# Performance work log

Hardware: AMD Instinct MI355X
Metric: run time of the kernel (lower is better)

The kernel has to match this reference:

```python
import jax, jax.numpy as jnp
import numpy as np

B, T, E, H = 4, 4096, 1024, 16
D = E // H          # per-head hidden_size in fla LinearAttention (num_heads=1)
CH = 64             # fused-chunk chunk size


def setup_inputs() -> dict:
    key = jax.random.key(0)
    k1, k2, k3, k4, k5 = jax.random.split(key, 5)
    s = 1.0 / np.sqrt(D).astype(np.float32)
    x = jax.random.normal(k1, (B, T, E), dtype=jnp.float32)
    Wq = jax.random.normal(k2, (D, D), dtype=jnp.float32) * s
    Wk = jax.random.normal(k3, (D, D), dtype=jnp.float32) * s
    Wv = jax.random.normal(k4, (D, D), dtype=jnp.float32) * s
    Wo = jax.random.normal(k5, (D, D), dtype=jnp.float32) * s
    return {"x": x, "Wq": Wq, "Wk": Wk, "Wv": Wv, "Wo": Wo}


def _phi(x):
    # fla 'elu' feature map: elu(x) + 1 (positive features)
    return jax.nn.elu(x) + 1.0


def _linear_attn_fused_chunk(q, k, v):
    # q,k,v: [B,H,T,D]; causal linear attention via chunked recurrence.
    b, h, t, d = q.shape
    n = t // CH
    # [N, B, H, CH, D] so scan runs over chunks
    qc = q.reshape(b, h, n, CH, d).transpose(2, 0, 1, 3, 4)
    kc = k.reshape(b, h, n, CH, d).transpose(2, 0, 1, 3, 4)
    vc = v.reshape(b, h, n, CH, d).transpose(2, 0, 1, 3, 4)
    mask = jnp.tril(jnp.ones((CH, CH), dtype=q.dtype))  # causal, diag inclusive

    def step(S, inp):
        qi, ki, vi = inp                                   # [B,H,CH,D]
        attn = jnp.einsum('bhck,bhek->bhce', qi, ki) * mask  # intra-chunk scores
        o_intra = jnp.einsum('bhce,bhed->bhcd', attn, vi)
        o_inter = jnp.einsum('bhck,bhkd->bhcd', qi, S)       # past-state term
        S_new = S + jnp.einsum('bhck,bhcd->bhkd', ki, vi)    # state update
        return S_new, o_intra + o_inter

    S0 = jnp.zeros((b, h, d, d), dtype=q.dtype)
    _, oc = jax.lax.scan(step, S0, (qc, kc, vc))           # oc: [N,B,H,CH,D]
    return oc.transpose(1, 2, 0, 3, 4).reshape(b, h, t, d)


def reference(x, Wq, Wk, Wv, Wo):
    # split outer heads: [B,T,E] -> [B,H,T,D]
    xh = x.reshape(B, T, H, D).transpose(0, 2, 1, 3)
    # shared [D,D] projections (fla LinearAttention with num_heads=1), tied elu feature map on q,k
    q = _phi(jnp.einsum('bhtd,de->bhte', xh, Wq))
    k = _phi(jnp.einsum('bhtd,de->bhte', xh, Wk))
    v = jnp.einsum('bhtd,de->bhte', xh, Wv)
    o = _linear_attn_fused_chunk(q, k, v)                  # no feature-map norm, identity output norm
    o = jnp.einsum('bhtd,de->bhte', o, Wo)
    return o.transpose(0, 2, 1, 3).reshape(B, T, E)
```

## Files before the change

### kernel.cpp

```cpp
#include <hip/hip_runtime.h>
#include <cstdint>
#include <cstddef>

constexpr int Bc = 4, Tc = 4096, Ec = 1024, Hc = 16, Dc = 64, CHc = 64;
constexpr int NSEG = 16;
constexpr int SEGT = Tc / NSEG;
constexpr int NCHUNK = SEGT / CHc;
constexpr int LP = 72;

typedef __attribute__((ext_vector_type(8))) short short8;
typedef __attribute__((ext_vector_type(4))) float f32x4;

__device__ __forceinline__ unsigned short f2bf(float f) {
  union { float f; unsigned int u; } v; v.f = f;
  return (unsigned short)((v.u + 0x7FFFu + ((v.u >> 16) & 1u)) >> 16);
}
__device__ __forceinline__ unsigned int pk2(float lo, float hi) {
  return ((unsigned int)f2bf(hi) << 16) | (unsigned int)f2bf(lo);
}
__device__ __forceinline__ float bf2f(unsigned short u) {
  union { unsigned int u; float f; } v; v.u = ((unsigned int)u) << 16;
  return v.f;
}
__device__ __forceinline__ float phi_elu1(float x) {
  return x > 0.f ? x + 1.f : __expf(x);
}
__device__ __forceinline__ short8 ld8(const unsigned short* p) {
  return *reinterpret_cast<const short8*>(p);
}
__device__ __forceinline__ short8 pk8(float4 a, float4 b) {
  union { unsigned int u[4]; short8 s; } r;
  r.u[0] = pk2(a.x, a.y); r.u[1] = pk2(a.z, a.w);
  r.u[2] = pk2(b.x, b.y); r.u[3] = pk2(b.z, b.w);
  return r.s;
}
__device__ __forceinline__ void st4(unsigned short* p, float v0, float v1, float v2, float v3) {
  union { unsigned int u[2]; uint2 t; } r;
  r.u[0] = pk2(v0, v1); r.u[1] = pk2(v2, v3);
  *reinterpret_cast<uint2*>(p) = r.t;
}

#define MFMA(a, b, c) __builtin_amdgcn_mfma_f32_16x16x32_bf16((a), (b), (c), 0, 0, 0)

__global__ void prep_weights(const float* __restrict__ Wq, const float* __restrict__ Wk,
                             const float* __restrict__ Wv, const float* __restrict__ Wo,
                             unsigned short* __restrict__ wbuf) {
  int gid = blockIdx.x * 256 + threadIdx.x;
  int m = gid >> 12, i = gid & 4095, r = i >> 6, c = i & 63;
  if (m == 0) {
    wbuf[i] = f2bf(Wq[c * 64 + r]);
  } else if (m == 1) {
    wbuf[4096 + i] = f2bf(Wk[c * 64 + r]);
  } else {
    float acc = 0.f;
    for (int g = 0; g < 64; ++g) acc += Wv[c * 64 + g] * Wo[g * 64 + r];
    wbuf[8192 + i] = f2bf(acc);
  }
}

__global__ __launch_bounds__(256, 3) void pass1_kvseg(
    const float* __restrict__ x, const unsigned short* __restrict__ wbuf,
    float* __restrict__ kvseg) {
  __shared__ unsigned short s_kT[64 * LP];
  __shared__ unsigned short s_vT[64 * LP];
  const int tid = threadIdx.x, w = tid >> 6, lane = tid & 63, lr = lane & 15, lq = lane >> 4;
  const int bh = blockIdx.x, sg = blockIdx.y, b = bh >> 4, h = bh & 15;
  const float* xbase = x + ((size_t)b * Tc + (size_t)sg * SEGT) * Ec + h * Dc;
  const unsigned short* wkT = wbuf + 4096;
  const unsigned short* wvoT = wbuf + 8192;
  const f32x4 Z = {0.f, 0.f, 0.f, 0.f};

  short8 bwk[4][2], bwv[4][2];
#pragma unroll
  for (int c = 0; c < 4; ++c)
#pragma unroll
    for (int kk = 0; kk < 2; ++kk) {
      bwk[c][kk] = ld8(wkT + (c * 16 + lr) * 64 + kk * 32 + lq * 8);
      bwv[c][kk] = ld8(wvoT + (c * 16 + lr) * 64 + kk * 32 + lq * 8);
    }

  const float* xr = xbase + (size_t)(w * 16 + lr) * Ec + lq * 8;
  float4 p0 = ((const float4*)xr)[0], p1 = ((const float4*)xr)[1];
  float4 p2 = ((const float4*)(xr + 32))[0], p3 = ((const float4*)(xr + 32))[1];

  f32x4 sacc[4] = {Z, Z, Z, Z};
#pragma unroll
  for (int ci = 0; ci < NCHUNK; ++ci) {
    short8 xa0 = pk8(p0, p1), xa1 = pk8(p2, p3);
    if (ci < NCHUNK - 1) {
      const float* nr = xbase + (size_t)((ci + 1) * CHc + w * 16 + lr) * Ec + lq * 8;
      p0 = ((const float4*)nr)[0]; p1 = ((const float4*)nr)[1];
      p2 = ((const float4*)(nr + 32))[0]; p3 = ((const float4*)(nr + 32))[1];
    }
    f32x4 ak[4] = {Z, Z, Z, Z}, av[4] = {Z, Z, Z, Z};
#pragma unroll
    for (int c = 0; c < 4; ++c) {
      ak[c] = MFMA(xa0, bwk[c][0], ak[c]); ak[c] = MFMA(xa1, bwk[c][1], ak[c]);
      av[c] = MFMA(xa0, bwv[c][0], av[c]); av[c] = MFMA(xa1, bwv[c][1], av[c]);
    }
#pragma unroll
    for (int c = 0; c < 4; ++c) {
      int o = (c * 16 + lr) * LP + w * 16 + lq * 4;
      st4(&s_kT[o], phi_elu1(ak[c][0]), phi_elu1(ak[c][1]), phi_elu1(ak[c][2]), phi_elu1(ak[c][3]));
      st4(&s_vT[o], av[c][0], av[c][1], av[c][2], av[c][3]);
    }
    __syncthreads();
    short8 akt0 = ld8(&s_kT[(w * 16 + lr) * LP + lq * 8]);
    short8 akt1 = ld8(&s_kT[(w * 16 + lr) * LP + 32 + lq * 8]);
#pragma unroll
    for (int c = 0; c < 4; ++c) {
      sacc[c] = MFMA(akt0, ld8(&s_vT[(c * 16 + lr) * LP + lq * 8]), sacc[c]);
      sacc[c] = MFMA(akt1, ld8(&s_vT[(c * 16 + lr) * LP + 32 + lq * 8]), sacc[c]);
    }
    __syncthreads();
  }
  float* dst = kvseg + ((size_t)(bh * NSEG + sg)) * 4096;
#pragma unroll
  for (int c = 0; c < 4; ++c)
#pragma unroll
    for (int j = 0; j < 4; ++j)
      dst[(w * 16 + lq * 4 + j) * 64 + c * 16 + lr] = sacc[c][j];
}

__global__ __launch_bounds__(256) void pass2_prefix(const float* __restrict__ kvseg,
                                                    unsigned short* __restrict__ sprefix) {
  const int bh = blockIdx.x, tile = blockIdx.y;
  const int e = tile * 1024 + threadIdx.x * 4;
  const float* src = kvseg + (size_t)bh * NSEG * 4096 + e;
  unsigned short* dst = sprefix + (size_t)bh * NSEG * 4096 + e;
  float4 vals[NSEG];
#pragma unroll
  for (int s = 0; s < NSEG; ++s) vals[s] = *(const float4*)(src + (size_t)s * 4096);
  float a0 = 0.f, a1 = 0.f, a2 = 0.f, a3 = 0.f;
#pragma unroll
  for (int s = 0; s < NSEG; ++s) {
    union { unsigned int u[2]; uint2 t; } r;
    r.u[0] = pk2(a0, a1); r.u[1] = pk2(a2, a3);
    *reinterpret_cast<uint2*>(dst + (size_t)s * 4096) = r.t;
    a0 += vals[s].x; a1 += vals[s].y; a2 += vals[s].z; a3 += vals[s].w;
  }
}

__global__ __launch_bounds__(256, 2) void pass3_main(
    const float* __restrict__ x, const unsigned short* __restrict__ wbuf,
    const unsigned short* __restrict__ sprefix, float* __restrict__ out) {
  __shared__ unsigned short s_x [64 * LP];
  __shared__ unsigned short s_q [64 * LP];
  __shared__ unsigned short s_k [64 * LP];
  __shared__ unsigned short s_kT[64 * LP];
  __shared__ unsigned short s_vT[64 * LP];
  __shared__ unsigned short s_Sb[64 * LP];
  __shared__ unsigned short s_at[64 * LP];

  const int tid = threadIdx.x, w = tid >> 6, lane = tid & 63, lr = lane & 15, lq = lane >> 4;
  const int bh = blockIdx.x, sg = blockIdx.y, b = bh >> 4, h = bh & 15;
  const float* xbase = x + ((size_t)b * Tc + (size_t)sg * SEGT) * Ec + h * Dc;
  float* obase = out + ((size_t)b * Tc + (size_t)sg * SEGT) * Ec + h * Dc;
  const unsigned short* wqT = wbuf;
  const unsigned short* wkT = wbuf + 4096;
  const unsigned short* wvoT = wbuf + 8192;
  const unsigned short* Sg = sprefix + ((size_t)(bh * NSEG + sg)) * 4096;
  const int sr = tid >> 2, sc = tid & 3;
  const f32x4 Z = {0.f, 0.f, 0.f, 0.f};

  f32x4 sacc[4];
#pragma unroll
  for (int c = 0; c < 4; ++c)
#pragma unroll
    for (int j = 0; j < 4; ++j)
      sacc[c][j] = bf2f(Sg[(w * 16 + lq * 4 + j) * 64 + c * 16 + lr]);

  short8 awq[2], awk[2], bwk[4][2], bwv[4][2];
#pragma unroll
  for (int kk = 0; kk < 2; ++kk) {
    awq[kk] = ld8(wqT + (w * 16 + lr) * 64 + kk * 32 + lq * 8);
    awk[kk] = ld8(wkT + (w * 16 + lr) * 64 + kk * 32 + lq * 8);
  }
#pragma unroll
  for (int c = 0; c < 4; ++c)
#pragma unroll
    for (int kk = 0; kk < 2; ++kk) {
      bwk[c][kk] = ld8(wkT + (c * 16 + lr) * 64 + kk * 32 + lq * 8);
      bwv[c][kk] = ld8(wvoT + (c * 16 + lr) * 64 + kk * 32 + lq * 8);
    }

  {
    const float4* xf = (const float4*)(xbase + (size_t)sr * Ec + sc * 16);
    float4 f0 = xf[0], f1 = xf[1], f2 = xf[2], f3 = xf[3];
    *(short8*)&s_x[sr * LP + sc * 16] = pk8(f0, f1);
    *(short8*)&s_x[sr * LP + sc * 16 + 8] = pk8(f2, f3);
  }
  __syncthreads();

#pragma unroll
  for (int ci = 0; ci < NCHUNK; ++ci) {
    float4 pf0, pf1, pf2, pf3;
    if (ci < NCHUNK - 1) {
      const float4* xf = (const float4*)(xbase + (size_t)((ci + 1) * CHc + sr) * Ec + sc * 16);
      pf0 = xf[0]; pf1 = xf[1]; pf2 = xf[2]; pf3 = xf[3];
    }

    short8 xb[4][2];
#pragma unroll
    for (int c = 0; c < 4; ++c) {
      xb[c][0] = ld8(&s_x[(c * 16 + lr) * LP + lq * 8]);
      xb[c][1] = ld8(&s_x[(c * 16 + lr) * LP + 32 + lq * 8]);
    }
    short8 xw0 = ld8(&s_x[(w * 16 + lr) * LP + lq * 8]);
    short8 xw1 = ld8(&s_x[(w * 16 + lr) * LP + 32 + lq * 8]);
#pragma unroll
    for (int c = 0; c < 4; ++c)
      st4(&s_Sb[(c * 16 + lr) * LP + w * 16 + lq * 4], sacc[c][0], sacc[c][1], sacc[c][2], sacc[c][3]);

    f32x4 aqt[4] = {Z, Z, Z, Z}, akt[4] = {Z, Z, Z, Z}, ack[4] = {Z, Z, Z, Z}, acv[4] = {Z, Z, Z, Z};
#pragma unroll
    for (int c = 0; c < 4; ++c) {
      aqt[c] = MFMA(awq[0], xb[c][0], aqt[c]); aqt[c] = MFMA(awq[1], xb[c][1], aqt[c]);
      akt[c] = MFMA(awk[0], xb[c][0], akt[c]); akt[c] = MFMA(awk[1], xb[c][1], akt[c]);
      ack[c] = MFMA(xw0, bwk[c][0], ack[c]);   ack[c] = MFMA(xw1, bwk[c][1], ack[c]);
      acv[c] = MFMA(xw0, bwv[c][0], acv[c]);   acv[c] = MFMA(xw1, bwv[c][1], acv[c]);
    }
#pragma unroll
    for (int c = 0; c < 4; ++c) {
      int o = (c * 16 + lr) * LP + w * 16 + lq * 4;
      st4(&s_q [o], phi_elu1(aqt[c][0]), phi_elu1(aqt[c][1]), phi_elu1(aqt[c][2]), phi_elu1(aqt[c][3]));
      st4(&s_k [o], phi_elu1(akt[c][0]), phi_elu1(akt[c][1]), phi_elu1(akt[c][2]), phi_elu1(akt[c][3]));
      st4(&s_kT[o], phi_elu1(ack[c][0]), phi_elu1(ack[c][1]), phi_elu1(ack[c][2]), phi_elu1(ack[c][3]));
      st4(&s_vT[o], acv[c][0], acv[c][1], acv[c][2], acv[c][3]);
    }
    __syncthreads();

    short8 a_q0 = ld8(&s_q [(w * 16 + lr) * LP + lq * 8]);
    short8 a_q1 = ld8(&s_q [(w * 16 + lr) * LP + 32 + lq * 8]);
    short8 a_k0 = ld8(&s_k [(w * 16 + lr) * LP + lq * 8]);
    short8 a_k1 = ld8(&s_k [(w * 16 + lr) * LP + 32 + lq * 8]);
    short8 a_t0 = ld8(&s_kT[(w * 16 + lr) * LP + lq * 8]);
    short8 a_t1 = ld8(&s_kT[(w * 16 + lr) * LP + 32 + lq * 8]);
    f32x4 aat[4] = {Z, Z, Z, Z}, ao[4] = {Z, Z, Z, Z};
#pragma unroll
    for (int c = 0; c < 4; ++c) {
      const int br = (c * 16 + lr) * LP;
      aat[c]  = MFMA(a_k0, ld8(&s_q [br + lq * 8]), aat[c]);
      aat[c]  = MFMA(a_k1, ld8(&s_q [br + 32 + lq * 8]), aat[c]);
      ao[c]   = MFMA(a_q0, ld8(&s_Sb[br + lq * 8]), ao[c]);
      ao[c]   = MFMA(a_q1, ld8(&s_Sb[br + 32 + lq * 8]), ao[c]);
      sacc[c] = MFMA(a_t0, ld8(&s_vT[br + lq * 8]), sacc[c]);
      sacc[c] = MFMA(a_t1, ld8(&s_vT[br + 32 + lq * 8]), sacc[c]);
    }
#pragma unroll
    for (int c = 0; c < 4; ++c) {
      int t = c * 16 + lr, tp = w * 16 + lq * 4;
      float m0 = (tp + 0 <= t) ? aat[c][0] : 0.f;
      float m1 = (tp + 1 <= t) ? aat[c][1] : 0.f;
      float m2 = (tp + 2 <= t) ? aat[c][2] : 0.f;
      float m3 = (tp + 3 <= t) ? aat[c][3] : 0.f;
      st4(&s_at[t * LP + tp], m0, m1, m2, m3);
    }
    __syncthreads();

    short8 a_a0 = ld8(&s_at[(w * 16 + lr) * LP + lq * 8]);
    short8 a_a1 = ld8(&s_at[(w * 16 + lr) * LP + 32 + lq * 8]);
#pragma unroll
    for (int c = 0; c < 4; ++c) {
      const int br = (c * 16 + lr) * LP;
      ao[c] = MFMA(a_a0, ld8(&s_vT[br + lq * 8]), ao[c]);
      ao[c] = MFMA(a_a1, ld8(&s_vT[br + 32 + lq * 8]), ao[c]);
    }
    float* orow = obase + (size_t)(ci * CHc) * Ec;
#pragma unroll
    for (int c = 0; c < 4; ++c)
#pragma unroll
      for (int j = 0; j < 4; ++j)
        orow[(size_t)(w * 16 + lq * 4 + j) * Ec + c * 16 + lr] = ao[c][j];
    if (ci < NCHUNK - 1) {
      *(short8*)&s_x[sr * LP + sc * 16] = pk8(pf0, pf1);
      *(short8*)&s_x[sr * LP + sc * 16 + 8] = pk8(pf2, pf3);
    }
    __syncthreads();
  }
}

extern "C" void kernel_launch(void* const* d_in, const int* in_sizes, int n_in,
                              void* d_out, int out_size, void* d_ws, size_t ws_size,
                              hipStream_t stream) {
  const float* x  = (const float*)d_in[0];
  const float* Wq = (const float*)d_in[1];
  const float* Wk = (const float*)d_in[2];
  const float* Wv = (const float*)d_in[3];
  const float* Wo = (const float*)d_in[4];
  float* out = (float*)d_out;

  unsigned short* wbuf = (unsigned short*)d_ws;
  float* kvseg = (float*)((char*)d_ws + 32768);
  unsigned short* sprefix = (unsigned short*)((char*)d_ws + 32768 + (size_t)16 * 1024 * 1024);

  prep_weights<<<dim3(48), dim3(256), 0, stream>>>(Wq, Wk, Wv, Wo, wbuf);
  pass1_kvseg<<<dim3(64, NSEG), dim3(256), 0, stream>>>(x, wbuf, kvseg);
  pass2_prefix<<<dim3(64, 4), dim3(256), 0, stream>>>(kvseg, sprefix);
  pass3_main<<<dim3(64, NSEG), dim3(256), 0, stream>>>(x, wbuf, sprefix, out);
}
```

Baseline: 79.52 us.

## Swizzle LDS tiles, reuse x buffer for scores, cheaper bf16 pack, restructure weight prep

Replaces the padded 72-stride LDS layout with an unpadded 128-byte-row XOR swizzle, which shrinks LDS per block. Pass3 reuses s_x for the masked score tile, dropping one buffer and raising the occupancy hint from 2 to 3 blocks. The bf16 conversion drops tie-to-even and uses plain round-half-up. Weight prep now stages Wv and Wo in shared memory and runs 16 blocks instead of 48. The risks are a small rounding difference and added address arithmetic for the swizzle.

```diff
diff --git a/kernel.cpp b/kernel.cpp
--- a/kernel.cpp
+++ b/kernel.cpp
@@ -6,17 +6,21 @@
 constexpr int NSEG = 16;
 constexpr int SEGT = Tc / NSEG;
 constexpr int NCHUNK = SEGT / CHc;
-constexpr int LP = 72;
 
 typedef __attribute__((ext_vector_type(8))) short short8;
 typedef __attribute__((ext_vector_type(4))) float f32x4;
+
+__device__ __forceinline__ unsigned short* sws(unsigned short* b, int row, int colbyte) {
+  return (unsigned short*)((char*)b + (row << 7) + (colbyte ^ ((row & 7) << 4)));
+}
 
 __device__ __forceinline__ unsigned short f2bf(float f) {
   union { float f; unsigned int u; } v; v.f = f;
   return (unsigned short)((v.u + 0x7FFFu + ((v.u >> 16) & 1u)) >> 16);
 }
 __device__ __forceinline__ unsigned int pk2(float lo, float hi) {
-  return ((unsigned int)f2bf(hi) << 16) | (unsigned int)f2bf(lo);
+  union { float f; unsigned int u; } a, b; a.f = lo; b.f = hi;
+  return ((a.u + 0x8000u) >> 16) | ((b.u + 0x8000u) & 0xFFFF0000u);
 }
 __device__ __forceinline__ float bf2f(unsigned short u) {
   union { unsigned int u; float f; } v; v.u = ((unsigned int)u) << 16;
@@ -35,34 +39,39 @@
   return r.s;
 }
 __device__ __forceinline__ void st4(unsigned short* p, float v0, float v1, float v2, float v3) {
-  union { unsigned int u[2]; uint2 t; } r;
-  r.u[0] = pk2(v0, v1); r.u[1] = pk2(v2, v3);
-  *reinterpret_cast<uint2*>(p) = r.t;
+  uint2 t; t.x = pk2(v0, v1); t.y = pk2(v2, v3);
+  *reinterpret_cast<uint2*>(p) = t;
 }
 
 #define MFMA(a, b, c) __builtin_amdgcn_mfma_f32_16x16x32_bf16((a), (b), (c), 0, 0, 0)
 
-__global__ void prep_weights(const float* __restrict__ Wq, const float* __restrict__ Wk,
-                             const float* __restrict__ Wv, const float* __restrict__ Wo,
-                             unsigned short* __restrict__ wbuf) {
-  int gid = blockIdx.x * 256 + threadIdx.x;
-  int m = gid >> 12, i = gid & 4095, r = i >> 6, c = i & 63;
-  if (m == 0) {
-    wbuf[i] = f2bf(Wq[c * 64 + r]);
-  } else if (m == 1) {
-    wbuf[4096 + i] = f2bf(Wk[c * 64 + r]);
-  } else {
-    float acc = 0.f;
-    for (int g = 0; g < 64; ++g) acc += Wv[c * 64 + g] * Wo[g * 64 + r];
-    wbuf[8192 + i] = f2bf(acc);
-  }
+__global__ __launch_bounds__(256) void prep_weights(
+    const float* __restrict__ Wq, const float* __restrict__ Wk,
+    const float* __restrict__ Wv, const float* __restrict__ Wo,
+    unsigned short* __restrict__ wbuf) {
+  __shared__ float s_wvT[4096];
+  __shared__ float s_wo[4096];
+  const int tid = threadIdx.x;
+  const int i = blockIdx.x * 256 + tid;
+  for (int j = tid; j < 4096; j += 256) {
+    s_wvT[(j & 63) * 64 + (j >> 6)] = Wv[j];
+    s_wo[j] = Wo[j];
+  }
+  __syncthreads();
+  const int r = i >> 6, c = i & 63;
+  wbuf[c * 64 + r] = f2bf(Wq[i]);
+  wbuf[4096 + c * 64 + r] = f2bf(Wk[i]);
+  float acc = 0.f;
+  for (int g = 0; g < 64; ++g)
+    acc += s_wvT[g * 64 + c] * s_wo[g * 64 + r];
+  wbuf[8192 + i] = f2bf(acc);
 }
 
 __global__ __launch_bounds__(256, 3) void pass1_kvseg(
     const float* __restrict__ x, const unsigned short* __restrict__ wbuf,
     float* __restrict__ kvseg) {
-  __shared__ unsigned short s_kT[64 * LP];
-  __shared__ unsigned short s_vT[64 * LP];
+  __shared__ unsigned short s_kT[4096];
+  __shared__ unsigned short s_vT[4096];
   const int tid = threadIdx.x, w = tid >> 6, lane = tid & 63, lr = lane & 15, lq = lane >> 4;
   const int bh = blockIdx.x, sg = blockIdx.y, b = bh >> 4, h = bh & 15;
   const float* xbase = x + ((size_t)b * Tc + (size_t)sg * SEGT) * Ec + h * Dc;
@@ -100,17 +109,19 @@
     }
 #pragma unroll
     for (int c = 0; c < 4; ++c) {
-      int o = (c * 16 + lr) * LP + w * 16 + lq * 4;
-      st4(&s_kT[o], phi_elu1(ak[c][0]), phi_elu1(ak[c][1]), phi_elu1(ak[c][2]), phi_elu1(ak[c][3]));
-      st4(&s_vT[o], av[c][0], av[c][1], av[c][2], av[c][3]);
-    }
-    __syncthreads();
-    short8 akt0 = ld8(&s_kT[(w * 16 + lr) * LP + lq * 8]);
-    short8 akt1 = ld8(&s_kT[(w * 16 + lr) * LP + 32 + lq * 8]);
-#pragma unroll
-    for (int c = 0; c < 4; ++c) {
-      sacc[c] = MFMA(akt0, ld8(&s_vT[(c * 16 + lr) * LP + lq * 8]), sacc[c]);
-      sacc[c] = MFMA(akt1, ld8(&s_vT[(c * 16 + lr) * LP + 32 + lq * 8]), sacc[c]);
+      unsigned short* pk_ = sws(s_kT, c * 16 + lr, w * 32 + lq * 8);
+      unsigned short* pv_ = sws(s_vT, c * 16 + lr, w * 32 + lq * 8);
+      st4(pk_, phi_elu1(ak[c][0]), phi_elu1(ak[c][1]), phi_elu1(ak[c][2]), phi_elu1(ak[c][3]));
+      st4(pv_, av[c][0], av[c][1], av[c][2], av[c][3]);
+    }
+    __syncthreads();
+
+    short8 akt0 = ld8(sws(s_kT, w * 16 + lr, lq * 16));
+    short8 akt1 = ld8(sws(s_kT, w * 16 + lr, 64 + lq * 16));
+#pragma unroll
+    for (int c = 0; c < 4; ++c) {
+      sacc[c] = MFMA(akt0, ld8(sws(s_vT, c * 16 + lr, lq * 16)), sacc[c]);
+      sacc[c] = MFMA(akt1, ld8(sws(s_vT, c * 16 + lr, 64 + lq * 16)), sacc[c]);
     }
     __syncthreads();
   }
@@ -134,23 +145,21 @@
   float a0 = 0.f, a1 = 0.f, a2 = 0.f, a3 = 0.f;
 #pragma unroll
   for (int s = 0; s < NSEG; ++s) {
-    union { unsigned int u[2]; uint2 t; } r;
-    r.u[0] = pk2(a0, a1); r.u[1] = pk2(a2, a3);
-    *reinterpret_cast<uint2*>(dst + (size_t)s * 4096) = r.t;
+    uint2 t; t.x = pk2(a0, a1); t.y = pk2(a2, a3);
+    *reinterpret_cast<uint2*>(dst + (size_t)s * 4096) = t;
     a0 += vals[s].x; a1 += vals[s].y; a2 += vals[s].z; a3 += vals[s].w;
   }
 }
 
-__global__ __launch_bounds__(256, 2) void pass3_main(
+__global__ __launch_bounds__(256, 3) void pass3_main(
     const float* __restrict__ x, const unsigned short* __restrict__ wbuf,
     const unsigned short* __restrict__ sprefix, float* __restrict__ out) {
-  __shared__ unsigned short s_x [64 * LP];
-  __shared__ unsigned short s_q [64 * LP];
-  __shared__ unsigned short s_k [64 * LP];
-  __shared__ unsigned short s_kT[64 * LP];
-  __shared__ unsigned short s_vT[64 * LP];
-  __shared__ unsigned short s_Sb[64 * LP];
-  __shared__ unsigned short s_at[64 * LP];
+  __shared__ unsigned short s_x [4096];
+  __shared__ unsigned short s_q [4096];
+  __shared__ unsigned short s_k [4096];
+  __shared__ unsigned short s_kT[4096];
+  __shared__ unsigned short s_vT[4096];
+  __shared__ unsigned short s_Sb[4096];
 
   const int tid = threadIdx.x, w = tid >> 6, lane = tid & 63, lr = lane & 15, lq = lane >> 4;
   const int bh = blockIdx.x, sg = blockIdx.y, b = bh >> 4, h = bh & 15;
@@ -187,8 +196,8 @@
   {
     const float4* xf = (const float4*)(xbase + (size_t)sr * Ec + sc * 16);
     float4 f0 = xf[0], f1 = xf[1], f2 = xf[2], f3 = xf[3];
-    *(short8*)&s_x[sr * LP + sc * 16] = pk8(f0, f1);
-    *(short8*)&s_x[sr * LP + sc * 16 + 8] = pk8(f2, f3);
+    *(short8*)sws(s_x, sr, sc * 32) = pk8(f0, f1);
+    *(short8*)sws(s_x, sr, sc * 32 + 16) = pk8(f2, f3);
   }
   __syncthreads();
 
@@ -203,14 +212,14 @@
     short8 xb[4][2];
 #pragma unroll
     for (int c = 0; c < 4; ++c) {
-      xb[c][0] = ld8(&s_x[(c * 16 + lr) * LP + lq * 8]);
-      xb[c][1] = ld8(&s_x[(c * 16 + lr) * LP + 32 + lq * 8]);
-    }
-    short8 xw0 = ld8(&s_x[(w * 16 + lr) * LP + lq * 8]);
-    short8 xw1 = ld8(&s_x[(w * 16 + lr) * LP + 32 + lq * 8]);
+      xb[c][0] = ld8(sws(s_x, c * 16 + lr, lq * 16));
+      xb[c][1] = ld8(sws(s_x, c * 16 + lr, 64 + lq * 16));
+    }
+    short8 xw0 = ld8(sws(s_x, w * 16 + lr, lq * 16));
+    short8 xw1 = ld8(sws(s_x, w * 16 + lr, 64 + lq * 16));
 #pragma unroll
     for (int c = 0; c < 4; ++c)
-      st4(&s_Sb[(c * 16 + lr) * LP + w * 16 + lq * 4], sacc[c][0], sacc[c][1], sacc[c][2], sacc[c][3]);
+      st4(sws(s_Sb, c * 16 + lr, w * 32 + lq * 8), sacc[c][0], sacc[c][1], sacc[c][2], sacc[c][3]);
 
     f32x4 aqt[4] = {Z, Z, Z, Z}, akt[4] = {Z, Z, Z, Z}, ack[4] = {Z, Z, Z, Z}, acv[4] = {Z, Z, Z, Z};
 #pragma unroll
@@ -222,30 +231,30 @@
     }
 #pragma unroll
     for (int c = 0; c < 4; ++c) {
-      int o = (c * 16 + lr) * LP + w * 16 + lq * 4;
-      st4(&s_q [o], phi_elu1(aqt[c][0]), phi_elu1(aqt[c][1]), phi_elu1(aqt[c][2]), phi_elu1(aqt[c][3]));
-      st4(&s_k [o], phi_elu1(akt[c][0]), phi_elu1(akt[c][1]), phi_elu1(akt[c][2]), phi_elu1(akt[c][3]));
-      st4(&s_kT[o], phi_elu1(ack[c][0]), phi_elu1(ack[c][1]), phi_elu1(ack[c][2]), phi_elu1(ack[c][3]));
-      st4(&s_vT[o], acv[c][0], acv[c][1], acv[c][2], acv[c][3]);
-    }
-    __syncthreads();
-
-    short8 a_q0 = ld8(&s_q [(w * 16 + lr) * LP + lq * 8]);
-    short8 a_q1 = ld8(&s_q [(w * 16 + lr) * LP + 32 + lq * 8]);
-    short8 a_k0 = ld8(&s_k [(w * 16 + lr) * LP + lq * 8]);
-    short8 a_k1 = ld8(&s_k [(w * 16 + lr) * LP + 32 + lq * 8]);
-    short8 a_t0 = ld8(&s_kT[(w * 16 + lr) * LP + lq * 8]);
-    short8 a_t1 = ld8(&s_kT[(w * 16 + lr) * LP + 32 + lq * 8]);
+      const int row = c * 16 + lr, cb = w * 32 + lq * 8;
+      st4(sws(s_q, row, cb), phi_elu1(aqt[c][0]), phi_elu1(aqt[c][1]), phi_elu1(aqt[c][2]), phi_elu1(aqt[c][3]));
+      st4(sws(s_k, row, cb), phi_elu1(akt[c][0]), phi_elu1(akt[c][1]), phi_elu1(akt[c][2]), phi_elu1(akt[c][3]));
+      st4(sws(s_kT, row, cb), phi_elu1(ack[c][0]), phi_elu1(ack[c][1]), phi_elu1(ack[c][2]), phi_elu1(ack[c][3]));
+      st4(sws(s_vT, row, cb), acv[c][0], acv[c][1], acv[c][2], acv[c][3]);
+    }
+    __syncthreads();
+
+    short8 a_q0 = ld8(sws(s_q, w * 16 + lr, lq * 16));
+    short8 a_q1 = ld8(sws(s_q, w * 16 + lr, 64 + lq * 16));
+    short8 a_k0 = ld8(sws(s_k, w * 16 + lr, lq * 16));
+    short8 a_k1 = ld8(sws(s_k, w * 16 + lr, 64 + lq * 16));
+    short8 a_t0 = ld8(sws(s_kT, w * 16 + lr, lq * 16));
+    short8 a_t1 = ld8(sws(s_kT, w * 16 + lr, 64 + lq * 16));
     f32x4 aat[4] = {Z, Z, Z, Z}, ao[4] = {Z, Z, Z, Z};
 #pragma unroll
     for (int c = 0; c < 4; ++c) {
-      const int br = (c * 16 + lr) * LP;
-      aat[c]  = MFMA(a_k0, ld8(&s_q [br + lq * 8]), aat[c]);
-      aat[c]  = MFMA(a_k1, ld8(&s_q [br + 32 + lq * 8]), aat[c]);
-      ao[c]   = MFMA(a_q0, ld8(&s_Sb[br + lq * 8]), ao[c]);
-      ao[c]   = MFMA(a_q1, ld8(&s_Sb[br + 32 + lq * 8]), ao[c]);
-      sacc[c] = MFMA(a_t0, ld8(&s_vT[br + lq * 8]), sacc[c]);
-      sacc[c] = MFMA(a_t1, ld8(&s_vT[br + 32 + lq * 8]), sacc[c]);
+      const int row = c * 16 + lr;
+      aat[c]  = MFMA(a_k0, ld8(sws(s_q, row, lq * 16)), aat[c]);
+      aat[c]  = MFMA(a_k1, ld8(sws(s_q, row, 64 + lq * 16)), aat[c]);
+      ao[c]   = MFMA(a_q0, ld8(sws(s_Sb, row, lq * 16)), ao[c]);
+      ao[c]   = MFMA(a_q1, ld8(sws(s_Sb, row, 64 + lq * 16)), ao[c]);
+      sacc[c] = MFMA(a_t0, ld8(sws(s_vT, row, lq * 16)), sacc[c]);
+      sacc[c] = MFMA(a_t1, ld8(sws(s_vT, row, 64 + lq * 16)), sacc[c]);
     }
 #pragma unroll
     for (int c = 0; c < 4; ++c) {
@@ -254,17 +263,17 @@
       float m1 = (tp + 1 <= t) ? aat[c][1] : 0.f;
       float m2 = (tp + 2 <= t) ? aat[c][2] : 0.f;
       float m3 = (tp + 3 <= t) ? aat[c][3] : 0.f;
-      st4(&s_at[t * LP + tp], m0, m1, m2, m3);
-    }
-    __syncthreads();
-
-    short8 a_a0 = ld8(&s_at[(w * 16 + lr) * LP + lq * 8]);
-    short8 a_a1 = ld8(&s_at[(w * 16 + lr) * LP + 32 + lq * 8]);
-#pragma unroll
-    for (int c = 0; c < 4; ++c) {
-      const int br = (c * 16 + lr) * LP;
-      ao[c] = MFMA(a_a0, ld8(&s_vT[br + lq * 8]), ao[c]);
-      ao[c] = MFMA(a_a1, ld8(&s_vT[br + 32 + lq * 8]), ao[c]);
+      st4(sws(s_x, t, tp * 2), m0, m1, m2, m3);
+    }
+    __syncthreads();
+
+    short8 a_a0 = ld8(sws(s_x, w * 16 + lr, lq * 16));
+    short8 a_a1 = ld8(sws(s_x, w * 16 + lr, 64 + lq * 16));
+#pragma unroll
+    for (int c = 0; c < 4; ++c) {
+      const int row = c * 16 + lr;
+      ao[c] = MFMA(a_a0, ld8(sws(s_vT, row, lq * 16)), ao[c]);
+      ao[c] = MFMA(a_a1, ld8(sws(s_vT, row, 64 + lq * 16)), ao[c]);
     }
     float* orow = obase + (size_t)(ci * CHc) * Ec;
 #pragma unroll
@@ -273,8 +282,8 @@
       for (int j = 0; j < 4; ++j)
         orow[(size_t)(w * 16 + lq * 4 + j) * Ec + c * 16 + lr] = ao[c][j];
     if (ci < NCHUNK - 1) {
-      *(short8*)&s_x[sr * LP + sc * 16] = pk8(pf0, pf1);
-      *(short8*)&s_x[sr * LP + sc * 16 + 8] = pk8(pf2, pf3);
+      *(short8*)sws(s_x, sr, sc * 32) = pk8(pf0, pf1);
+      *(short8*)sws(s_x, sr, sc * 32 + 16) = pk8(pf2, pf3);
     }
     __syncthreads();
   }
@@ -294,7 +303,7 @@
   float* kvseg = (float*)((char*)d_ws + 32768);
   unsigned short* sprefix = (unsigned short*)((char*)d_ws + 32768 + (size_t)16 * 1024 * 1024);
 
-  prep_weights<<<dim3(48), dim3(256), 0, stream>>>(Wq, Wk, Wv, Wo, wbuf);
+  prep_weights<<<dim3(16), dim3(256), 0, stream>>>(Wq, Wk, Wv, Wo, wbuf);
   pass1_kvseg<<<dim3(64, NSEG), dim3(256), 0, stream>>>(x, wbuf, kvseg);
   pass2_prefix<<<dim3(64, 4), dim3(256), 0, stream>>>(kvseg, sprefix);
   pass3_main<<<dim3(64, NSEG), dim3(256), 0, stream>>>(x, wbuf, sprefix, out);
```

Result: slower. 132.3 us (+66.4%).
